# Performance work log

Hardware: AMD Instinct MI355X
Metric: run time of the kernel (lower is better)

Reference implementation:

```python
import jax, jax.numpy as jnp
import numpy as np

N, E, IN_DIM, HID, HEADS, N_CLASSES, N_GRAPHS = 50000, 800000, 128, 64, 4, 16, 64
NEG_SLOPE = 0.2


def setup_inputs() -> dict:
    key = jax.random.key(0)
    ks = jax.random.split(key, 12)
    s = 0.1
    return {
        "x": jax.random.normal(ks[0], (N, IN_DIM), jnp.float32),
        "edge_index": jax.random.randint(ks[1], (2, E), 0, N, jnp.int32),
        "batch": jnp.sort(jax.random.randint(ks[2], (N,), 0, N_GRAPHS, jnp.int32)),
        "W1": jax.random.normal(ks[3], (IN_DIM, HEADS * HID), jnp.float32) * s,
        "a_src1": jax.random.normal(ks[4], (HEADS, HID), jnp.float32) * s,
        "a_dst1": jax.random.normal(ks[5], (HEADS, HID), jnp.float32) * s,
        "b1": jnp.zeros((HEADS * HID,), jnp.float32),
        "W2": jax.random.normal(ks[6], (HEADS * HID, HID), jnp.float32) * s,
        "a_src2": jax.random.normal(ks[7], (1, HID), jnp.float32) * s,
        "a_dst2": jax.random.normal(ks[8], (1, HID), jnp.float32) * s,
        "b2": jnp.zeros((HID,), jnp.float32),
        "fcW": jax.random.normal(ks[9], (HID, N_CLASSES), jnp.float32) * s,
        "fcb": jnp.zeros((N_CLASSES,), jnp.float32),
    }


def gat_conv(x, edge_index, W, a_src, a_dst, bias, concat):
    # PyG GATConv (eval mode): add self loops, per-head linear, additive attention,
    # segment softmax over incoming edges of each destination node, scatter-add.
    n = x.shape[0]
    heads, d = a_src.shape
    h = (x @ W).reshape(n, heads, d)                      # [n, H, d]
    asrc = jnp.einsum('nhd,hd->nh', h, a_src)             # [n, H]
    adst = jnp.einsum('nhd,hd->nh', h, a_dst)             # [n, H]
    loops = jnp.arange(n, dtype=edge_index.dtype)
    src = jnp.concatenate([edge_index[0], loops])         # message sources j
    dst = jnp.concatenate([edge_index[1], loops])         # targets i
    e = jax.nn.leaky_relu(asrc[src] + adst[dst], NEG_SLOPE)  # [E+n, H]
    m = jax.ops.segment_max(e, dst, num_segments=n)
    p = jnp.exp(e - m[dst])
    s = jax.ops.segment_sum(p, dst, num_segments=n)
    alpha = p / (s[dst] + 1e-16)                          # [E+n, H]
    msg = h[src] * alpha[:, :, None]                      # [E+n, H, d]
    out = jax.ops.segment_sum(msg, dst, num_segments=n)   # [n, H, d]
    out = out.reshape(n, heads * d) if concat else out.mean(axis=1)
    return out + bias


def reference(x, edge_index, batch, W1, a_src1, a_dst1, b1, W2, a_src2, a_dst2, b2, fcW, fcb):
    h = jax.nn.elu(gat_conv(x, edge_index, W1, a_src1, a_dst1, b1, True))
    h = gat_conv(h, edge_index, W2, a_src2, a_dst2, b2, False)
    # global_mean_pool over graph ids
    cnt = jax.ops.segment_sum(jnp.ones((h.shape[0],), h.dtype), batch, num_segments=N_GRAPHS)
    pooled = jax.ops.segment_sum(h, batch, num_segments=N_GRAPHS) / jnp.maximum(cnt, 1.0)[:, None]
    return pooled @ fcW + fcb
```

## Files before the change

kernel.cpp:

```cpp
#include <hip/hip_runtime.h>
#include <hip/hip_bf16.h>
#include <hip/hip_fp8.h>


#define Nn 50000
#define Ed 800000
#define NEG 0.2f
#define CAP 64
#define GBLK 782
#define SBLK 3125
#define TOTB 3907
#define NB4 12500

typedef __attribute__((ext_vector_type(8))) short short8;
typedef __attribute__((ext_vector_type(4))) float f32x4;
typedef __attribute__((ext_vector_type(2))) float f32x2;

#if defined(__has_builtin)
#if __has_builtin(__builtin_amdgcn_cvt_pk_f32_fp8) && __has_builtin(__builtin_amdgcn_cvt_pk_fp8_f32)
#define FP8_FAST 1
#endif
#endif
#ifndef FP8_FAST
#define FP8_FAST 0
#endif

__device__ __forceinline__ float lrelu(float x){ return fmaxf(x, NEG*x); }
__device__ __forceinline__ float bf2f(unsigned short u){ return __uint_as_float((unsigned)u << 16); }
__device__ __forceinline__ unsigned short f2bf(float f){
    __hip_bfloat16 b = __float2bfloat16(f);
    return *reinterpret_cast<unsigned short*>(&b);
}
__device__ __forceinline__ short f2bfs(float f){ return (short)f2bf(f); }

__device__ __forceinline__ unsigned char f2fp8(float f){
#if FP8_FAST
    int v = __builtin_amdgcn_cvt_pk_fp8_f32(f, f, 0, false);
    return (unsigned char)(v & 0xff);
#else
    __hip_fp8_e4m3 t(f);
    return (unsigned char)t.__x;
#endif
}

__device__ __forceinline__ float4 fp8x4_to_f32(unsigned int v){
#if FP8_FAST
    f32x2 lo = __builtin_amdgcn_cvt_pk_f32_fp8((int)v, false);
    f32x2 hi = __builtin_amdgcn_cvt_pk_f32_fp8((int)v, true);
    return make_float4(lo[0], lo[1], hi[0], hi[1]);
#else
    __hip_fp8_e4m3 t0, t1, t2, t3;
    t0.__x = (unsigned char)(v);
    t1.__x = (unsigned char)(v >> 8);
    t2.__x = (unsigned char)(v >> 16);
    t3.__x = (unsigned char)(v >> 24);
    return make_float4((float)t0, (float)t1, (float)t2, (float)t3);
#endif
}

__global__ void k_init(int* __restrict__ cnt,
                       const float* __restrict__ W1, const float* __restrict__ W2,
                       unsigned short* __restrict__ W1s, unsigned short* __restrict__ W2s){
    if (blockIdx.x < 196){
        int i = blockIdx.x*256 + threadIdx.x;
        if (i < Nn) cnt[i] = 0;
    } else {
        int t = (blockIdx.x - 196)*256 + threadIdx.x;
        if (t < 32768){
            int j = t & 7, lane = (t>>3) & 63, ks = (t>>9) & 3, nt = t>>11;
            W1s[t] = f2bf(W1[(ks*32 + (lane>>4)*8 + j)*256 + nt*16 + (lane&15)]);
        }
        if (t < 16384){
            int j = t & 7, lane = (t>>3) & 63, ks = (t>>9) & 7, nt = t>>12;
            W2s[t] = f2bf(W2[(ks*32 + (lane>>4)*8 + j)*64 + nt*16 + (lane&15)]);
        }
    }
}

__global__ __launch_bounds__(256) void k_scatter_gemm1(
        const float* __restrict__ x, const unsigned short* __restrict__ W1s,
        const float* __restrict__ a_src, const float* __restrict__ a_dst,
        unsigned char* __restrict__ h1f8,
        float* __restrict__ asrc, float* __restrict__ adst,
        const int* __restrict__ esrc, const int* __restrict__ edst,
        int* __restrict__ cnt, int* __restrict__ csr){
    int b = blockIdx.x;
    if (b % 5 != 0){
        int e = (b - b/5 - 1)*256 + threadIdx.x;
        int d = edst[e];
        int slot = atomicAdd(&cnt[d], 1);
        if (slot < CAP) csr[d*CAP + slot] = esrc[e];
        return;
    }
    int wv = (b/5)*4 + (threadIdx.x>>6);
    int lane = threadIdx.x & 63;
    int m0 = wv*16;
    if (m0 >= Nn) return;
    int quad = lane >> 4, col = lane & 15;
    int mrow = m0 + col;
    f32x4 acc[16] = {};
    const float* ap0 = &x[(size_t)mrow*128 + quad*8];
    #pragma unroll
    for (int ks = 0; ks < 4; ks++){
        float4 a0 = *(const float4*)(ap0 + ks*32);
        float4 a1 = *(const float4*)(ap0 + ks*32 + 4);
        short8 af;
        af[0]=f2bfs(a0.x); af[1]=f2bfs(a0.y); af[2]=f2bfs(a0.z); af[3]=f2bfs(a0.w);
        af[4]=f2bfs(a1.x); af[5]=f2bfs(a1.y); af[6]=f2bfs(a1.z); af[7]=f2bfs(a1.w);
        #pragma unroll
        for (int nt = 0; nt < 16; nt++){
            short8 bf = *(const short8*)&W1s[(size_t)(nt*4+ks)*512 + lane*8];
            acc[nt] = __builtin_amdgcn_mfma_f32_16x16x32_bf16(af, bf, acc[nt], 0, 0, 0);
        }
    }
    unsigned char* outp = &h1f8[(size_t)(m0 + quad*4)*256 + col];
    #pragma unroll
    for (int nt = 0; nt < 16; nt++)
        #pragma unroll
        for (int r = 0; r < 4; r++)
            outp[(size_t)r*256 + nt*16] = f2fp8(acc[nt][r]);
    float asf[16], adf[16];
    #pragma unroll
    for (int nt = 0; nt < 16; nt++){
        asf[nt] = a_src[nt*16 + col];
        adf[nt] = a_dst[nt*16 + col];
    }
    #pragma unroll
    for (int h = 0; h < 4; h++){
        #pragma unroll
        for (int r = 0; r < 4; r++){
            float ps = acc[4*h+0][r]*asf[4*h+0] + acc[4*h+1][r]*asf[4*h+1]
                     + acc[4*h+2][r]*asf[4*h+2] + acc[4*h+3][r]*asf[4*h+3];
            float pd = acc[4*h+0][r]*adf[4*h+0] + acc[4*h+1][r]*adf[4*h+1]
                     + acc[4*h+2][r]*adf[4*h+2] + acc[4*h+3][r]*adf[4*h+3];
            #pragma unroll
            for (int m = 1; m < 16; m <<= 1){ ps += __shfl_xor(ps, m); pd += __shfl_xor(pd, m); }
            if (col == h*4 + r){
                int n = m0 + quad*4 + r;
                asrc[n*4 + h] = ps;
                adst[n*4 + h] = pd;
            }
        }
    }
}

__global__ __launch_bounds__(256) void k_aggr1(const unsigned char* __restrict__ h1f8,
                                               const float* __restrict__ asrc, const float* __restrict__ adst,
                                               const int* __restrict__ cnt, const int* __restrict__ csr,
                                               const float* __restrict__ b1, unsigned short* __restrict__ g1){
    int w = threadIdx.x >> 6, lane = threadIdx.x & 63;
    int i = blockIdx.x*4 + w;
    int hh = lane >> 4;
    float ad = adst[i*4 + hh];
    float as = asrc[i*4 + hh];
    float p = __expf(lrelu(as + ad));
    unsigned int hv = *(const unsigned int*)&h1f8[(size_t)i*256 + 4*lane];
    float4 hd = fp8x4_to_f32(hv);
    float acc0 = p*hd.x, acc1 = p*hd.y, acc2 = p*hd.z, acc3 = p*hd.w;
    float ssum = p;
    const int* row = &csr[i*CAP];
    int end = min(cnt[i], CAP);
    int j = 0;
    for (; j + 3 < end; j += 4){
        int s0 = row[j], s1 = row[j+1], s2 = row[j+2], s3 = row[j+3];
        float a0 = asrc[s0*4 + hh];
        float a1 = asrc[s1*4 + hh];
        float a2 = asrc[s2*4 + hh];
        float a3 = asrc[s3*4 + hh];
        unsigned int v0 = *(const unsigned int*)&h1f8[(size_t)s0*256 + 4*lane];
        unsigned int v1 = *(const unsigned int*)&h1f8[(size_t)s1*256 + 4*lane];
        unsigned int v2 = *(const unsigned int*)&h1f8[(size_t)s2*256 + 4*lane];
        unsigned int v3 = *(const unsigned int*)&h1f8[(size_t)s3*256 + 4*lane];
        float q0 = __expf(lrelu(a0 + ad));
        float q1 = __expf(lrelu(a1 + ad));
        float q2 = __expf(lrelu(a2 + ad));
        float q3 = __expf(lrelu(a3 + ad));
        float4 d0 = fp8x4_to_f32(v0);
        float4 d1 = fp8x4_to_f32(v1);
        float4 d2 = fp8x4_to_f32(v2);
        float4 d3 = fp8x4_to_f32(v3);
        acc0 += q0*d0.x + q1*d1.x + q2*d2.x + q3*d3.x;
        acc1 += q0*d0.y + q1*d1.y + q2*d2.y + q3*d3.y;
        acc2 += q0*d0.z + q1*d1.z + q2*d2.z + q3*d3.z;
        acc3 += q0*d0.w + q1*d1.w + q2*d2.w + q3*d3.w;
        ssum += q0 + q1 + q2 + q3;
    }
    for (; j < end; j++){
        int s = row[j];
        float a = asrc[s*4 + hh];
        unsigned int v = *(const unsigned int*)&h1f8[(size_t)s*256 + 4*lane];
        float q = __expf(lrelu(a + ad));
        float4 d = fp8x4_to_f32(v);
        acc0 += q*d.x; acc1 += q*d.y; acc2 += q*d.z; acc3 += q*d.w;
        ssum += q;
    }
    float inv = 1.0f/(ssum + 1e-16f);
    float4 b4 = *(const float4*)&b1[4*lane];
    float o0 = acc0*inv + b4.x;
    float o1 = acc1*inv + b4.y;
    float o2 = acc2*inv + b4.z;
    float o3 = acc3*inv + b4.w;
    ushort4 o;
    o.x = f2bf(o0 > 0.f ? o0 : expm1f(o0));
    o.y = f2bf(o1 > 0.f ? o1 : expm1f(o1));
    o.z = f2bf(o2 > 0.f ? o2 : expm1f(o2));
    o.w = f2bf(o3 > 0.f ? o3 : expm1f(o3));
    *(ushort4*)&g1[(size_t)i*256 + 4*lane] = o;
}

__global__ __launch_bounds__(256) void k_gemm2(const unsigned short* __restrict__ g1b,
                                               const unsigned short* __restrict__ W2s,
                                               const float* __restrict__ a_src, const float* __restrict__ a_dst,
                                               unsigned short* __restrict__ h2b,
                                               float* __restrict__ asrc, float* __restrict__ adst){
    int wv = blockIdx.x*4 + (threadIdx.x>>6);
    int lane = threadIdx.x & 63;
    int m0 = wv*16;
    if (m0 >= Nn) return;
    int quad = lane >> 4, col = lane & 15;
    int mrow = m0 + col;
    f32x4 acc[4] = {};
    const unsigned short* ap0 = &g1b[(size_t)mrow*256 + quad*8];
    #pragma unroll
    for (int ks = 0; ks < 8; ks++){
        short8 af = *(const short8*)(ap0 + ks*32);
        #pragma unroll
        for (int nt = 0; nt < 4; nt++){
            short8 bf = *(const short8*)&W2s[(size_t)(nt*8+ks)*512 + lane*8];
            acc[nt] = __builtin_amdgcn_mfma_f32_16x16x32_bf16(af, bf, acc[nt], 0, 0, 0);
        }
    }
    unsigned short* outp = &h2b[(size_t)(m0 + quad*4)*64 + col];
    #pragma unroll
    for (int nt = 0; nt < 4; nt++)
        #pragma unroll
        for (int r = 0; r < 4; r++)
            outp[(size_t)r*64 + nt*16] = f2bf(acc[nt][r]);
    float asf[4], adf[4];
    #pragma unroll
    for (int nt = 0; nt < 4; nt++){
        asf[nt] = a_src[nt*16 + col];
        adf[nt] = a_dst[nt*16 + col];
    }
    #pragma unroll
    for (int r = 0; r < 4; r++){
        float ps = acc[0][r]*asf[0] + acc[1][r]*asf[1] + acc[2][r]*asf[2] + acc[3][r]*asf[3];
        float pd = acc[0][r]*adf[0] + acc[1][r]*adf[1] + acc[2][r]*adf[2] + acc[3][r]*adf[3];
        #pragma unroll
        for (int m = 1; m < 16; m <<= 1){ ps += __shfl_xor(ps, m); pd += __shfl_xor(pd, m); }
        if (col == r){
            int n = m0 + quad*4 + r;
            asrc[n] = ps;
            adst[n] = pd;
        }
    }
}

__global__ __launch_bounds__(256) void k_aggr2(const unsigned short* __restrict__ h2,
                                               const float* __restrict__ asrc, const float* __restrict__ adst,
                                               const int* __restrict__ cnt, const int* __restrict__ csr,
                                               unsigned short* __restrict__ g2){
    int w = threadIdx.x >> 6, lane = threadIdx.x & 63;
    int i = blockIdx.x*4 + w;
    float ad = adst[i];
    float p = __expf(lrelu(asrc[i] + ad));
    float acc = p * bf2f(h2[(size_t)i*64 + lane]);
    float ss = p;
    const int* row = &csr[i*CAP];
    int end = min(cnt[i], CAP);
    int j = 0;
    for (; j + 3 < end; j += 4){
        int s0 = row[j], s1 = row[j+1], s2 = row[j+2], s3 = row[j+3];
        float a0 = asrc[s0], a1 = asrc[s1], a2 = asrc[s2], a3 = asrc[s3];
        unsigned short v0 = h2[(size_t)s0*64 + lane];
        unsigned short v1 = h2[(size_t)s1*64 + lane];
        unsigned short v2 = h2[(size_t)s2*64 + lane];
        unsigned short v3 = h2[(size_t)s3*64 + lane];
        float q0 = __expf(lrelu(a0 + ad));
        float q1 = __expf(lrelu(a1 + ad));
        float q2 = __expf(lrelu(a2 + ad));
        float q3 = __expf(lrelu(a3 + ad));
        acc += q0*bf2f(v0) + q1*bf2f(v1) + q2*bf2f(v2) + q3*bf2f(v3);
        ss += q0 + q1 + q2 + q3;
    }
    for (; j < end; j++){
        int s = row[j];
        float q = __expf(lrelu(asrc[s] + ad));
        acc += q * bf2f(h2[(size_t)s*64 + lane]);
        ss += q;
    }
    g2[(size_t)i*64 + lane] = f2bf(acc/(ss + 1e-16f));
}

__global__ __launch_bounds__(256) void k_head(const unsigned short* __restrict__ g2,
                                              const int* __restrict__ batch,
                                              const float* __restrict__ b2,
                                              const float* __restrict__ fcW, const float* __restrict__ fcb,
                                              float* __restrict__ out){
    int g = blockIdx.x;
    int w = threadIdx.x >> 6, lane = threadIdx.x & 63;
    int lo = 0, hi = Nn;
    while (lo < hi){ int mid = (lo+hi)>>1; if (batch[mid] < g) lo = mid+1; else hi = mid; }
    int first = lo;
    lo = 0; hi = Nn;
    while (lo < hi){ int mid = (lo+hi)>>1; if (batch[mid] < g+1) lo = mid+1; else hi = mid; }
    int last = lo;
    float acc = 0.f;
    int n = first + w;
    for (; n + 4 < last; n += 8){
        acc += bf2f(g2[(size_t)n*64 + lane]);
        acc += bf2f(g2[(size_t)(n+4)*64 + lane]);
    }
    for (; n < last; n += 4) acc += bf2f(g2[(size_t)n*64 + lane]);
    __shared__ float part[4][64];
    part[w][lane] = acc;
    __syncthreads();
    if (w == 0){
        float tot = part[0][lane] + part[1][lane] + part[2][lane] + part[3][lane];
        float inv = 1.0f / fmaxf((float)(last - first), 1.0f);
        float val = tot*inv + b2[lane];
        #pragma unroll
        for (int c = 0; c < 16; c++){
            float t = val * fcW[lane*16 + c];
            #pragma unroll
            for (int m = 1; m < 64; m <<= 1) t += __shfl_xor(t, m);
            if (lane == 0) out[g*16 + c] = t + fcb[c];
        }
    }
}

extern "C" void kernel_launch(void* const* d_in, const int* in_sizes, int n_in,
                              void* d_out, int out_size, void* d_ws, size_t ws_size,
                              hipStream_t stream) {
    const float* x      = (const float*)d_in[0];
    const int*   ei     = (const int*)d_in[1];
    const int*   batch  = (const int*)d_in[2];
    const float* W1     = (const float*)d_in[3];
    const float* a_src1 = (const float*)d_in[4];
    const float* a_dst1 = (const float*)d_in[5];
    const float* b1     = (const float*)d_in[6];
    const float* W2     = (const float*)d_in[7];
    const float* a_src2 = (const float*)d_in[8];
    const float* a_dst2 = (const float*)d_in[9];
    const float* b2     = (const float*)d_in[10];
    const float* fcW    = (const float*)d_in[11];
    const float* fcb    = (const float*)d_in[12];
    float* out = (float*)d_out;

    char* ws = (char*)d_ws;
    size_t off = 0;
    auto carve = [&](size_t bytes)->void*{
        void* p = ws + off;
        off += (bytes + 255) & ~(size_t)255;
        return p;
    };
    int* cnt = (int*)carve((size_t)Nn*4);
    unsigned char*  h1f8 = (unsigned char*)carve((size_t)Nn*256);
    unsigned short* g1b  = (unsigned short*)carve((size_t)Nn*256*2);
    unsigned short* h2b  = (unsigned short*)carve((size_t)Nn*64*2);
    unsigned short* g2b  = (unsigned short*)carve((size_t)Nn*64*2);
    float* asrc1  = (float*)carve((size_t)Nn*4*4);
    float* adst1  = (float*)carve((size_t)Nn*4*4);
    float* asrc2  = (float*)carve((size_t)Nn*4);
    float* adst2  = (float*)carve((size_t)Nn*4);
    int*   csr    = (int*)carve((size_t)Nn*CAP*4);
    unsigned short* W1s = (unsigned short*)carve(32768*2);
    unsigned short* W2s = (unsigned short*)carve(16384*2);

    k_init<<<324, 256, 0, stream>>>(cnt, W1, W2, W1s, W2s);
    k_scatter_gemm1<<<TOTB, 256, 0, stream>>>(x, W1s, a_src1, a_dst1, h1f8, asrc1, adst1,
                                              ei, ei + Ed, cnt, csr);
    k_aggr1<<<NB4, 256, 0, stream>>>(h1f8, asrc1, adst1, cnt, csr, b1, g1b);
    k_gemm2<<<GBLK, 256, 0, stream>>>(g1b, W2s, a_src2, a_dst2, h2b, asrc2, adst2);
    k_aggr2<<<NB4, 256, 0, stream>>>(h2b, asrc2, adst2, cnt, csr, g2b);
    k_head<<<64, 256, 0, stream>>>(g2b, batch, b2, fcW, fcb, out);
}
```

Before: 268.1 us.

## Fuse layer-1 aggregation with layer-2 GEMM via shared-memory staging

Merges the layer-1 attention aggregation and the layer-2 MFMA GEMM into one kernel. Each 1024-thread block aggregates 16 nodes into shared memory, then one wave runs the 16x64 GEMM and attention projections from LDS. This removes the bf16 g1 global round trip (about 25 MB written and read) and one kernel launch. In exchange, 15 of 16 waves sit idle during the GEMM phase, and the larger blocks with a barrier may lower occupancy and leave the gather waves waiting.

Result: slower. 276.1 us (+3.0%).

```diff
diff --git a/kernel.cpp b/kernel.cpp
--- a/kernel.cpp
+++ b/kernel.cpp
@@ -10,6 +10,7 @@
 #define GBLK 782
 #define SBLK 3125
 #define TOTB 3907
+#define NB16 3125
 #define NB4 12500
 
 typedef __attribute__((ext_vector_type(8))) short short8;
@@ -144,12 +145,18 @@
     }
 }
 
-__global__ __launch_bounds__(256) void k_aggr1(const unsigned char* __restrict__ h1f8,
-                                               const float* __restrict__ asrc, const float* __restrict__ adst,
-                                               const int* __restrict__ cnt, const int* __restrict__ csr,
-                                               const float* __restrict__ b1, unsigned short* __restrict__ g1){
+__global__ __launch_bounds__(1024) void k_aggr1_gemm2(
+        const unsigned char* __restrict__ h1f8,
+        const float* __restrict__ asrc, const float* __restrict__ adst,
+        const int* __restrict__ cnt, const int* __restrict__ csr,
+        const float* __restrict__ b1,
+        const unsigned short* __restrict__ W2s,
+        const float* __restrict__ a_src2, const float* __restrict__ a_dst2,
+        unsigned short* __restrict__ h2b,
+        float* __restrict__ asrc2, float* __restrict__ adst2){
+    __shared__ unsigned short g1s[16][256];
     int w = threadIdx.x >> 6, lane = threadIdx.x & 63;
-    int i = blockIdx.x*4 + w;
+    int i = blockIdx.x*16 + w;
     int hh = lane >> 4;
     float ad = adst[i*4 + hh];
     float as = asrc[i*4 + hh];
@@ -205,29 +212,20 @@
     o.y = f2bf(o1 > 0.f ? o1 : expm1f(o1));
     o.z = f2bf(o2 > 0.f ? o2 : expm1f(o2));
     o.w = f2bf(o3 > 0.f ? o3 : expm1f(o3));
-    *(ushort4*)&g1[(size_t)i*256 + 4*lane] = o;
-}
-
-__global__ __launch_bounds__(256) void k_gemm2(const unsigned short* __restrict__ g1b,
-                                               const unsigned short* __restrict__ W2s,
-                                               const float* __restrict__ a_src, const float* __restrict__ a_dst,
-                                               unsigned short* __restrict__ h2b,
-                                               float* __restrict__ asrc, float* __restrict__ adst){
-    int wv = blockIdx.x*4 + (threadIdx.x>>6);
-    int lane = threadIdx.x & 63;
-    int m0 = wv*16;
-    if (m0 >= Nn) return;
+    *(ushort4*)&g1s[w][4*lane] = o;
+    __syncthreads();
+
+    if (threadIdx.x >= 64) return;
     int quad = lane >> 4, col = lane & 15;
-    int mrow = m0 + col;
-    f32x4 acc[4] = {};
-    const unsigned short* ap0 = &g1b[(size_t)mrow*256 + quad*8];
+    int m0 = blockIdx.x*16;
+    f32x4 accg[4] = {};
     #pragma unroll
     for (int ks = 0; ks < 8; ks++){
-        short8 af = *(const short8*)(ap0 + ks*32);
+        short8 af = *(const short8*)&g1s[col][ks*32 + quad*8];
         #pragma unroll
         for (int nt = 0; nt < 4; nt++){
             short8 bf = *(const short8*)&W2s[(size_t)(nt*8+ks)*512 + lane*8];
-            acc[nt] = __builtin_amdgcn_mfma_f32_16x16x32_bf16(af, bf, acc[nt], 0, 0, 0);
+            accg[nt] = __builtin_amdgcn_mfma_f32_16x16x32_bf16(af, bf, accg[nt], 0, 0, 0);
         }
     }
     unsigned short* outp = &h2b[(size_t)(m0 + quad*4)*64 + col];
@@ -235,23 +233,23 @@
     for (int nt = 0; nt < 4; nt++)
         #pragma unroll
         for (int r = 0; r < 4; r++)
-            outp[(size_t)r*64 + nt*16] = f2bf(acc[nt][r]);
+            outp[(size_t)r*64 + nt*16] = f2bf(accg[nt][r]);
     float asf[4], adf[4];
     #pragma unroll
     for (int nt = 0; nt < 4; nt++){
-        asf[nt] = a_src[nt*16 + col];
-        adf[nt] = a_dst[nt*16 + col];
+        asf[nt] = a_src2[nt*16 + col];
+        adf[nt] = a_dst2[nt*16 + col];
     }
     #pragma unroll
     for (int r = 0; r < 4; r++){
-        float ps = acc[0][r]*asf[0] + acc[1][r]*asf[1] + acc[2][r]*asf[2] + acc[3][r]*asf[3];
-        float pd = acc[0][r]*adf[0] + acc[1][r]*adf[1] + acc[2][r]*adf[2] + acc[3][r]*adf[3];
+        float ps = accg[0][r]*asf[0] + accg[1][r]*asf[1] + accg[2][r]*asf[2] + accg[3][r]*asf[3];
+        float pd = accg[0][r]*adf[0] + accg[1][r]*adf[1] + accg[2][r]*adf[2] + accg[3][r]*adf[3];
         #pragma unroll
         for (int m = 1; m < 16; m <<= 1){ ps += __shfl_xor(ps, m); pd += __shfl_xor(pd, m); }
         if (col == r){
             int n = m0 + quad*4 + r;
-            asrc[n] = ps;
-            adst[n] = pd;
+            asrc2[n] = ps;
+            adst2[n] = pd;
         }
     }
 }
@@ -356,7 +354,6 @@
     };
     int* cnt = (int*)carve((size_t)Nn*4);
     unsigned char*  h1f8 = (unsigned char*)carve((size_t)Nn*256);
-    unsigned short* g1b  = (unsigned short*)carve((size_t)Nn*256*2);
     unsigned short* h2b  = (unsigned short*)carve((size_t)Nn*64*2);
     unsigned short* g2b  = (unsigned short*)carve((size_t)Nn*64*2);
     float* asrc1  = (float*)carve((size_t)Nn*4*4);
@@ -370,8 +367,8 @@
     k_init<<<324, 256, 0, stream>>>(cnt, W1, W2, W1s, W2s);
     k_scatter_gemm1<<<TOTB, 256, 0, stream>>>(x, W1s, a_src1, a_dst1, h1f8, asrc1, adst1,
                                               ei, ei + Ed, cnt, csr);
-    k_aggr1<<<NB4, 256, 0, stream>>>(h1f8, asrc1, adst1, cnt, csr, b1, g1b);
-    k_gemm2<<<GBLK, 256, 0, stream>>>(g1b, W2s, a_src2, a_dst2, h2b, asrc2, adst2);
+    k_aggr1_gemm2<<<NB16, 1024, 0, stream>>>(h1f8, asrc1, adst1, cnt, csr, b1,
+                                             W2s, a_src2, a_dst2, h2b, asrc2, adst2);
     k_aggr2<<<NB4, 256, 0, stream>>>(h2b, asrc2, adst2, cnt, csr, g2b);
     k_head<<<64, 256, 0, stream>>>(g2b, batch, b2, fcW, fcb, out);
 }
```
